# Kernel optimization log

Measured on AMD Instinct MI355X. Metric: run time of the kernel, lower is better.

## Reference

```python
import jax, jax.numpy as jnp
import numpy as np
import math

B, L, H, NH = 2, 256, 512, 8
DH = H // NH


def setup_inputs() -> dict:
    key0 = jax.random.key(0)
    ks = jax.random.split(key0, 20)
    s = 0.02
    inp = {
        "key": jax.random.normal(ks[0], (B, L, H), jnp.float32),
        "query": jax.random.normal(ks[1], (B, L, H), jnp.float32),
        "value": jax.random.normal(ks[2], (B, L, H), jnp.float32),
        "seq_len": L // 2 + jax.random.randint(ks[3], (B,), 0, L // 2 + 1),
        "lex_num": 0,
        "pos_s": jax.random.randint(ks[4], (B, L), 0, L),
        "pos_e": jax.random.randint(ks[5], (B, L), 0, L),
        "rel_pos_embedding": jax.random.normal(ks[6], (B, L, L, H), jnp.float32),
        "Wk": jax.random.normal(ks[7], (H, H), jnp.float32) * s,
        "bk": jnp.zeros((H,), jnp.float32),
        "Wq": jax.random.normal(ks[8], (H, H), jnp.float32) * s,
        "bq": jnp.zeros((H,), jnp.float32),
        "Wv": jax.random.normal(ks[9], (H, H), jnp.float32) * s,
        "bv": jnp.zeros((H,), jnp.float32),
        "Wr": jax.random.normal(ks[10], (H, H), jnp.float32) * s,
        "br": jnp.zeros((H,), jnp.float32),
        "u": jax.random.normal(ks[11], (NH, DH), jnp.float32) * s,
        "v": jax.random.normal(ks[12], (NH, DH), jnp.float32) * s,
        "Wf": jax.random.normal(ks[13], (H, H), jnp.float32) * s,
        "bf": jnp.zeros((H,), jnp.float32),
    }
    return inp


def reference(key, query, value, seq_len, lex_num, pos_s, pos_e, rel_pos_embedding,
              Wk, bk, Wq, bq, Wv, bv, Wr, br, u, v, Wf, bf):
    b, sl = key.shape[0], key.shape[1]
    # projections (k/q/v/r_proj all True)
    k = key @ Wk + bk
    q = query @ Wq + bq
    val = value @ Wv + bv
    rel = rel_pos_embedding @ Wr + br            # [B,L,L,H]
    # split heads
    kh = k.reshape(b, sl, NH, DH).transpose(0, 2, 1, 3)    # [B,nh,L,dh]
    qh = q.reshape(b, sl, NH, DH).transpose(0, 2, 1, 3)
    vh = val.reshape(b, sl, NH, DH).transpose(0, 2, 1, 3)
    relh = rel.reshape(b, sl, sl, NH, DH)                   # [B,L,L,nh,dh]
    # A+C: (q + u) @ k^T
    q_u = qh + u[None, :, None, :]
    AC = jnp.einsum('bnid,bnjd->bnij', q_u, kh)
    # B+D: (q + v) . rel_pos per (i,j) pair
    q_v = qh + v[None, :, None, :]
    BD = jnp.einsum('bnid,bijnd->bnij', q_v, relh)
    scores = (AC + BD) / math.sqrt(DH)
    # mask padded keys: mask[b,j] = j < seq_len[b] + lex_num
    valid = jnp.arange(sl)[None, :] < (seq_len + lex_num)[:, None]   # [B,L]
    scores = jnp.where(valid[:, None, None, :], scores, -1e15)
    attn = jax.nn.softmax(scores, axis=-1)       # dropout p=0 -> identity
    out = jnp.einsum('bnij,bnjd->bnid', attn, vh)
    out = out.transpose(0, 2, 1, 3).reshape(b, sl, H)
    return out @ Wf + bf
```

## Files before the change

### kernel.cpp

```cpp
#include <hip/hip_runtime.h>
#include <math.h>


__global__ __launch_bounds__(256) void gemm512_k(
    const float* __restrict__ A0, const float* __restrict__ W0,
    const float* __restrict__ b0, float* __restrict__ C0,
    const float* __restrict__ A1, const float* __restrict__ W1,
    const float* __restrict__ b1, float* __restrict__ C1,
    const float* __restrict__ A2, const float* __restrict__ W2,
    const float* __restrict__ b2, float* __restrict__ C2) {
  const int z = blockIdx.z;
  const float* A    = (z == 0) ? A0 : (z == 1) ? A1 : A2;
  const float* W    = (z == 0) ? W0 : (z == 1) ? W1 : W2;
  const float* bias = (z == 0) ? b0 : (z == 1) ? b1 : b2;
  float* C          = (z == 0) ? C0 : (z == 1) ? C1 : C2;

  __shared__ float As[16][64];
  __shared__ float Bs[16][64];
  const int t  = threadIdx.x;
  const int tx = t & 15, ty = t >> 4;
  const int bm0 = blockIdx.y * 64, bn0 = blockIdx.x * 64;
  const int lm  = t >> 2;
  const int lkq = (t & 3) << 2;
  const int lk  = t >> 4;
  const int lnq = (t & 15) << 2;

  float acc[4][4] = {};
  for (int kt = 0; kt < 32; ++kt) {
    float4 a4 = *(const float4*)&A[(bm0 + lm) * 512 + kt * 16 + lkq];
    float4 b4 = *(const float4*)&W[(kt * 16 + lk) * 512 + bn0 + lnq];
    As[lkq + 0][lm] = a4.x;
    As[lkq + 1][lm] = a4.y;
    As[lkq + 2][lm] = a4.z;
    As[lkq + 3][lm] = a4.w;
    *(float4*)&Bs[lk][lnq] = b4;
    __syncthreads();
#pragma unroll
    for (int k = 0; k < 16; ++k) {
      float4 av = *(const float4*)&As[k][ty * 4];
      float4 bv = *(const float4*)&Bs[k][tx * 4];
      acc[0][0] = fmaf(av.x, bv.x, acc[0][0]);
      acc[0][1] = fmaf(av.x, bv.y, acc[0][1]);
      acc[0][2] = fmaf(av.x, bv.z, acc[0][2]);
      acc[0][3] = fmaf(av.x, bv.w, acc[0][3]);
      acc[1][0] = fmaf(av.y, bv.x, acc[1][0]);
      acc[1][1] = fmaf(av.y, bv.y, acc[1][1]);
      acc[1][2] = fmaf(av.y, bv.z, acc[1][2]);
      acc[1][3] = fmaf(av.y, bv.w, acc[1][3]);
      acc[2][0] = fmaf(av.z, bv.x, acc[2][0]);
      acc[2][1] = fmaf(av.z, bv.y, acc[2][1]);
      acc[2][2] = fmaf(av.z, bv.z, acc[2][2]);
      acc[2][3] = fmaf(av.z, bv.w, acc[2][3]);
      acc[3][0] = fmaf(av.w, bv.x, acc[3][0]);
      acc[3][1] = fmaf(av.w, bv.y, acc[3][1]);
      acc[3][2] = fmaf(av.w, bv.z, acc[3][2]);
      acc[3][3] = fmaf(av.w, bv.w, acc[3][3]);
    }
    __syncthreads();
  }
  float4 bb = *(const float4*)&bias[bn0 + tx * 4];
#pragma unroll
  for (int r = 0; r < 4; ++r) {
    float4 o;
    o.x = acc[r][0] + bb.x;
    o.y = acc[r][1] + bb.y;
    o.z = acc[r][2] + bb.z;
    o.w = acc[r][3] + bb.w;
    *(float4*)&C[(size_t)(bm0 + ty * 4 + r) * 512 + bn0 + tx * 4] = o;
  }
}

__global__ __launch_bounds__(256) void g_gemm_k(const float* __restrict__ q,
                                                const float* __restrict__ vbias,
                                                const float* __restrict__ Wr,
                                                float* __restrict__ g) {
  __shared__ float As[64][64];
  __shared__ float Bs[64][64];
  const int t   = threadIdx.x;
  const int bi0 = blockIdx.x * 64;
  const int eb  = blockIdx.y * 64;
  const int n   = blockIdx.z;
  const int row = t >> 2;
  const int dq  = (t & 3) << 4;
#pragma unroll
  for (int s = 0; s < 4; ++s) {
    int d = dq + s * 4;
    float4 a4 = *(const float4*)&q[(size_t)(bi0 + row) * 512 + n * 64 + d];
    float4 v4 = *(const float4*)&vbias[n * 64 + d];
    As[d + 0][row] = a4.x + v4.x;
    As[d + 1][row] = a4.y + v4.y;
    As[d + 2][row] = a4.z + v4.z;
    As[d + 3][row] = a4.w + v4.w;
    float4 b4 = *(const float4*)&Wr[(size_t)(eb + row) * 512 + n * 64 + d];
    Bs[d + 0][row] = b4.x;
    Bs[d + 1][row] = b4.y;
    Bs[d + 2][row] = b4.z;
    Bs[d + 3][row] = b4.w;
  }
  __syncthreads();
  const int tx = t & 15, ty = t >> 4;
  float acc[4][4] = {};
#pragma unroll 8
  for (int d = 0; d < 64; ++d) {
    float4 av = *(const float4*)&As[d][ty * 4];
    float4 bv = *(const float4*)&Bs[d][tx * 4];
    acc[0][0] = fmaf(av.x, bv.x, acc[0][0]);
    acc[0][1] = fmaf(av.x, bv.y, acc[0][1]);
    acc[0][2] = fmaf(av.x, bv.z, acc[0][2]);
    acc[0][3] = fmaf(av.x, bv.w, acc[0][3]);
    acc[1][0] = fmaf(av.y, bv.x, acc[1][0]);
    acc[1][1] = fmaf(av.y, bv.y, acc[1][1]);
    acc[1][2] = fmaf(av.y, bv.z, acc[1][2]);
    acc[1][3] = fmaf(av.y, bv.w, acc[1][3]);
    acc[2][0] = fmaf(av.z, bv.x, acc[2][0]);
    acc[2][1] = fmaf(av.z, bv.y, acc[2][1]);
    acc[2][2] = fmaf(av.z, bv.z, acc[2][2]);
    acc[2][3] = fmaf(av.z, bv.w, acc[2][3]);
    acc[3][0] = fmaf(av.w, bv.x, acc[3][0]);
    acc[3][1] = fmaf(av.w, bv.y, acc[3][1]);
    acc[3][2] = fmaf(av.w, bv.z, acc[3][2]);
    acc[3][3] = fmaf(av.w, bv.w, acc[3][3]);
  }
#pragma unroll
  for (int r = 0; r < 4; ++r) {
    float4 o = {acc[r][0], acc[r][1], acc[r][2], acc[r][3]};
    *(float4*)&g[((size_t)(bi0 + ty * 4 + r) * 8 + n) * 512 + eb + tx * 4] = o;
  }
}

__global__ __launch_bounds__(256) void score_k(
    const float* __restrict__ q, const float* __restrict__ kk,
    const float* __restrict__ g, const float* __restrict__ rpe,
    const float* __restrict__ u, const float* __restrict__ v,
    const float* __restrict__ br, const int* __restrict__ seq_len,
    const int* __restrict__ lex_num, float* __restrict__ scores) {
  const int bi = blockIdx.x;
  const int b = bi >> 8, i = bi & 255;
  const int lane = threadIdx.x & 63;
  const int w = threadIdx.x >> 6;
  const int grp = lane >> 3, sub = lane & 7;
  const int e0 = lane << 3;
  const int jblock = blockIdx.y * 128;
  const int jbase = jblock + w * 32;
  __shared__ float ac[8][128];
  __shared__ float cterm[8];
  const int limit = seq_len[b] + lex_num[0];

  float qu[8];
  {
    const float* qrow = q + (size_t)bi * 512 + e0;
    float4 q0 = *(const float4*)qrow;
    float4 q1 = *(const float4*)(qrow + 4);
    float4 u0 = *(const float4*)(u + e0);
    float4 u1 = *(const float4*)(u + e0 + 4);
    qu[0] = q0.x + u0.x; qu[1] = q0.y + u0.y; qu[2] = q0.z + u0.z; qu[3] = q0.w + u0.w;
    qu[4] = q1.x + u1.x; qu[5] = q1.y + u1.y; qu[6] = q1.z + u1.z; qu[7] = q1.w + u1.w;
  }
  for (int jj = 0; jj < 32; ++jj) {
    int j = jbase + jj;
    const float* krow = kk + (size_t)(b * 256 + j) * 512 + e0;
    float4 k0 = *(const float4*)krow;
    float4 k1 = *(const float4*)(krow + 4);
    float p = qu[0] * k0.x;
    p = fmaf(qu[1], k0.y, p);
    p = fmaf(qu[2], k0.z, p);
    p = fmaf(qu[3], k0.w, p);
    p = fmaf(qu[4], k1.x, p);
    p = fmaf(qu[5], k1.y, p);
    p = fmaf(qu[6], k1.z, p);
    p = fmaf(qu[7], k1.w, p);
    p += __shfl_xor(p, 1);
    p += __shfl_xor(p, 2);
    p += __shfl_xor(p, 4);
    if (sub == 0) ac[grp][j - jblock] = p;
  }
  if (w == 0) {
    const float* qrow = q + (size_t)bi * 512 + e0;
    float4 q0 = *(const float4*)qrow;
    float4 q1 = *(const float4*)(qrow + 4);
    float4 v0 = *(const float4*)(v + e0);
    float4 v1 = *(const float4*)(v + e0 + 4);
    float4 r0 = *(const float4*)(br + e0);
    float4 r1 = *(const float4*)(br + e0 + 4);
    float p = (q0.x + v0.x) * r0.x;
    p = fmaf(q0.y + v0.y, r0.y, p);
    p = fmaf(q0.z + v0.z, r0.z, p);
    p = fmaf(q0.w + v0.w, r0.w, p);
    p = fmaf(q1.x + v1.x, r1.x, p);
    p = fmaf(q1.y + v1.y, r1.y, p);
    p = fmaf(q1.z + v1.z, r1.z, p);
    p = fmaf(q1.w + v1.w, r1.w, p);
    p += __shfl_xor(p, 1);
    p += __shfl_xor(p, 2);
    p += __shfl_xor(p, 4);
    if (sub == 0) cterm[grp] = p;
  }
  __syncthreads();

  float gf[8][8];
#pragma unroll
  for (int n = 0; n < 8; ++n) {
    const float* grow = g + ((size_t)bi * 8 + n) * 512 + e0;
    float4 ga = *(const float4*)grow;
    float4 gb = *(const float4*)(grow + 4);
    gf[n][0] = ga.x; gf[n][1] = ga.y; gf[n][2] = ga.z; gf[n][3] = ga.w;
    gf[n][4] = gb.x; gf[n][5] = gb.y; gf[n][6] = gb.z; gf[n][7] = gb.w;
  }
  const int s1 = sub & 1, s2 = (sub >> 1) & 1, s4 = (sub >> 2) & 1;
  const float* rbase = rpe + (size_t)bi * 256 * 512;
#pragma unroll 2
  for (int jj = 0; jj < 32; ++jj) {
    int j = jbase + jj;
    const float* rrow = rbase + (size_t)j * 512 + e0;
    float4 r0 = *(const float4*)rrow;
    float4 r1 = *(const float4*)(rrow + 4);
    float a[8];
#pragma unroll
    for (int n = 0; n < 8; ++n) {
      float s = r0.x * gf[n][0];
      s = fmaf(r0.y, gf[n][1], s);
      s = fmaf(r0.z, gf[n][2], s);
      s = fmaf(r0.w, gf[n][3], s);
      s = fmaf(r1.x, gf[n][4], s);
      s = fmaf(r1.y, gf[n][5], s);
      s = fmaf(r1.z, gf[n][6], s);
      s = fmaf(r1.w, gf[n][7], s);
      a[n] = s;
    }
    float b0 = (s1 ? a[1] : a[0]) + __shfl_xor(s1 ? a[0] : a[1], 1);
    float b1 = (s1 ? a[3] : a[2]) + __shfl_xor(s1 ? a[2] : a[3], 1);
    float b2 = (s1 ? a[5] : a[4]) + __shfl_xor(s1 ? a[4] : a[5], 1);
    float b3 = (s1 ? a[7] : a[6]) + __shfl_xor(s1 ? a[6] : a[7], 1);
    float c0 = (s2 ? b1 : b0) + __shfl_xor(s2 ? b0 : b1, 2);
    float c1 = (s2 ? b3 : b2) + __shfl_xor(s2 ? b2 : b3, 2);
    float tot = (s4 ? c1 : c0) + __shfl_xor(s4 ? c0 : c1, 4);
    tot += __shfl_xor(tot, 8);
    tot += __shfl_xor(tot, 16);
    tot += __shfl_xor(tot, 32);
    if (lane < 8) {
      float val = (ac[lane][j - jblock] + cterm[lane] + tot) * 0.125f;
      if (j >= limit) val = -1e15f;
      scores[((size_t)(b * 8 + lane) * 256 + i) * 256 + j] = val;
    }
  }
}

__global__ __launch_bounds__(256) void softmax_pv_k(const float* __restrict__ scores,
                                                    const float* __restrict__ val,
                                                    float* __restrict__ ctx) {
  const int bi = blockIdx.x;
  const int b = bi >> 8, i = bi & 255;
  const int t = threadIdx.x;
  const int lane = t & 63, w = t >> 6;
  __shared__ float p_lds[8][256];
#pragma unroll
  for (int h = 0; h < 2; ++h) {
    const int n = w * 2 + h;
    const float* srow = scores + ((size_t)(b * 8 + n) * 256 + i) * 256;
    float x0 = srow[lane], x1 = srow[lane + 64], x2 = srow[lane + 128], x3 = srow[lane + 192];
    float m = fmaxf(fmaxf(x0, x1), fmaxf(x2, x3));
#pragma unroll
    for (int off = 1; off < 64; off <<= 1) m = fmaxf(m, __shfl_xor(m, off));
    float e0 = __expf(x0 - m), e1 = __expf(x1 - m), e2 = __expf(x2 - m), e3 = __expf(x3 - m);
    float s = e0 + e1 + e2 + e3;
#pragma unroll
    for (int off = 1; off < 64; off <<= 1) s += __shfl_xor(s, off);
    float inv = 1.0f / s;
    p_lds[n][lane] = e0 * inv;
    p_lds[n][lane + 64] = e1 * inv;
    p_lds[n][lane + 128] = e2 * inv;
    p_lds[n][lane + 192] = e3 * inv;
  }
  __syncthreads();
  const int c = t * 2;
  const int n = c >> 6;
  float2 acc = {0.f, 0.f};
  const float* vb = val + (size_t)b * 256 * 512 + c;
#pragma unroll 4
  for (int j = 0; j < 256; ++j) {
    float p = p_lds[n][j];
    float2 vv = *(const float2*)(vb + (size_t)j * 512);
    acc.x = fmaf(p, vv.x, acc.x);
    acc.y = fmaf(p, vv.y, acc.y);
  }
  *(float2*)&ctx[(size_t)bi * 512 + c] = acc;
}

extern "C" void kernel_launch(void* const* d_in, const int* in_sizes, int n_in,
                              void* d_out, int out_size, void* d_ws, size_t ws_size,
                              hipStream_t stream) {
  const float* key     = (const float*)d_in[0];
  const float* query   = (const float*)d_in[1];
  const float* value   = (const float*)d_in[2];
  const int* seq_len   = (const int*)d_in[3];
  const int* lex_num   = (const int*)d_in[4];
  const float* rpe     = (const float*)d_in[7];
  const float* Wk      = (const float*)d_in[8];
  const float* bk      = (const float*)d_in[9];
  const float* Wq      = (const float*)d_in[10];
  const float* bq      = (const float*)d_in[11];
  const float* Wv      = (const float*)d_in[12];
  const float* bv      = (const float*)d_in[13];
  const float* Wr      = (const float*)d_in[14];
  const float* br      = (const float*)d_in[15];
  const float* u       = (const float*)d_in[16];
  const float* v       = (const float*)d_in[17];
  const float* Wf      = (const float*)d_in[18];
  const float* bf      = (const float*)d_in[19];
  float* out = (float*)d_out;

  float* ws     = (float*)d_ws;
  float* q_ws   = ws;
  float* k_ws   = q_ws + 262144;
  float* val_ws = k_ws + 262144;
  float* g_ws   = val_ws + 262144;
  float* sc_ws  = g_ws + 2097152;
  float* ctx_ws = sc_ws + 1048576;

  dim3 blk(256);
  gemm512_k<<<dim3(8, 8, 3), blk, 0, stream>>>(query, Wq, bq, q_ws,
                                               key, Wk, bk, k_ws,
                                               value, Wv, bv, val_ws);
  g_gemm_k<<<dim3(8, 8, 8), blk, 0, stream>>>(q_ws, v, Wr, g_ws);
  score_k<<<dim3(512, 2), blk, 0, stream>>>(q_ws, k_ws, g_ws, rpe, u, v, br,
                                            seq_len, lex_num, sc_ws);
  softmax_pv_k<<<dim3(512), blk, 0, stream>>>(sc_ws, val_ws, ctx_ws);
  gemm512_k<<<dim3(8, 8, 1), blk, 0, stream>>>(ctx_ws, Wf, bf, out,
                                               ctx_ws, Wf, bf, out,
                                               ctx_ws, Wf, bf, out);
}
```

Measured before the change: 530.4 us.

## Fuse score, softmax and PV into one attention kernel; prefetch GEMM tiles

The score kernel and the softmax-PV kernel are merged into a single attn_k kernel per (b,i) row. Scores stay in shared memory instead of going out to global, and the q·k term is folded into the rel-pos reduction per head. The grid shrinks from 512x2 to 512 blocks, each handling all 256 keys, so there is less parallelism on the dominant rel_pos_embedding stream. The projection GEMM also register-prefetches the next k tile so global loads overlap the FMA loop.

```diff
diff --git a/kernel.cpp b/kernel.cpp
--- a/kernel.cpp
+++ b/kernel.cpp
@@ -26,15 +26,20 @@
   const int lnq = (t & 15) << 2;
 
   float acc[4][4] = {};
+  float4 a4 = *(const float4*)&A[(bm0 + lm) * 512 + lkq];
+  float4 b4 = *(const float4*)&W[lk * 512 + bn0 + lnq];
   for (int kt = 0; kt < 32; ++kt) {
-    float4 a4 = *(const float4*)&A[(bm0 + lm) * 512 + kt * 16 + lkq];
-    float4 b4 = *(const float4*)&W[(kt * 16 + lk) * 512 + bn0 + lnq];
     As[lkq + 0][lm] = a4.x;
     As[lkq + 1][lm] = a4.y;
     As[lkq + 2][lm] = a4.z;
     As[lkq + 3][lm] = a4.w;
     *(float4*)&Bs[lk][lnq] = b4;
     __syncthreads();
+    float4 a4n = a4, b4n = b4;
+    if (kt < 31) {
+      a4n = *(const float4*)&A[(bm0 + lm) * 512 + (kt + 1) * 16 + lkq];
+      b4n = *(const float4*)&W[((kt + 1) * 16 + lk) * 512 + bn0 + lnq];
+    }
 #pragma unroll
     for (int k = 0; k < 16; ++k) {
       float4 av = *(const float4*)&As[k][ty * 4];
@@ -57,6 +62,8 @@
       acc[3][3] = fmaf(av.w, bv.w, acc[3][3]);
     }
     __syncthreads();
+    a4 = a4n;
+    b4 = b4n;
   }
   float4 bb = *(const float4*)&bias[bn0 + tx * 4];
 #pragma unroll
@@ -128,21 +135,20 @@
   }
 }
 
-__global__ __launch_bounds__(256) void score_k(
+__global__ __launch_bounds__(256) void attn_k(
     const float* __restrict__ q, const float* __restrict__ kk,
     const float* __restrict__ g, const float* __restrict__ rpe,
     const float* __restrict__ u, const float* __restrict__ v,
     const float* __restrict__ br, const int* __restrict__ seq_len,
-    const int* __restrict__ lex_num, float* __restrict__ scores) {
+    const int* __restrict__ lex_num, const float* __restrict__ val,
+    float* __restrict__ ctx) {
   const int bi = blockIdx.x;
-  const int b = bi >> 8, i = bi & 255;
-  const int lane = threadIdx.x & 63;
-  const int w = threadIdx.x >> 6;
+  const int b = bi >> 8;
+  const int t = threadIdx.x;
+  const int lane = t & 63, w = t >> 6;
   const int grp = lane >> 3, sub = lane & 7;
   const int e0 = lane << 3;
-  const int jblock = blockIdx.y * 128;
-  const int jbase = jblock + w * 32;
-  __shared__ float ac[8][128];
+  __shared__ float sc[8][256];
   __shared__ float cterm[8];
   const int limit = seq_len[b] + lex_num[0];
 
@@ -156,23 +162,14 @@
     qu[0] = q0.x + u0.x; qu[1] = q0.y + u0.y; qu[2] = q0.z + u0.z; qu[3] = q0.w + u0.w;
     qu[4] = q1.x + u1.x; qu[5] = q1.y + u1.y; qu[6] = q1.z + u1.z; qu[7] = q1.w + u1.w;
   }
-  for (int jj = 0; jj < 32; ++jj) {
-    int j = jbase + jj;
-    const float* krow = kk + (size_t)(b * 256 + j) * 512 + e0;
-    float4 k0 = *(const float4*)krow;
-    float4 k1 = *(const float4*)(krow + 4);
-    float p = qu[0] * k0.x;
-    p = fmaf(qu[1], k0.y, p);
-    p = fmaf(qu[2], k0.z, p);
-    p = fmaf(qu[3], k0.w, p);
-    p = fmaf(qu[4], k1.x, p);
-    p = fmaf(qu[5], k1.y, p);
-    p = fmaf(qu[6], k1.z, p);
-    p = fmaf(qu[7], k1.w, p);
-    p += __shfl_xor(p, 1);
-    p += __shfl_xor(p, 2);
-    p += __shfl_xor(p, 4);
-    if (sub == 0) ac[grp][j - jblock] = p;
+  float gf[8][8];
+#pragma unroll
+  for (int n = 0; n < 8; ++n) {
+    const float* grow = g + ((size_t)bi * 8 + n) * 512 + e0;
+    float4 ga = *(const float4*)grow;
+    float4 gb = *(const float4*)(grow + 4);
+    gf[n][0] = ga.x; gf[n][1] = ga.y; gf[n][2] = ga.z; gf[n][3] = ga.w;
+    gf[n][4] = gb.x; gf[n][5] = gb.y; gf[n][6] = gb.z; gf[n][7] = gb.w;
   }
   if (w == 0) {
     const float* qrow = q + (size_t)bi * 512 + e0;
@@ -197,23 +194,26 @@
   }
   __syncthreads();
 
-  float gf[8][8];
-#pragma unroll
-  for (int n = 0; n < 8; ++n) {
-    const float* grow = g + ((size_t)bi * 8 + n) * 512 + e0;
-    float4 ga = *(const float4*)grow;
-    float4 gb = *(const float4*)(grow + 4);
-    gf[n][0] = ga.x; gf[n][1] = ga.y; gf[n][2] = ga.z; gf[n][3] = ga.w;
-    gf[n][4] = gb.x; gf[n][5] = gb.y; gf[n][6] = gb.z; gf[n][7] = gb.w;
-  }
   const int s1 = sub & 1, s2 = (sub >> 1) & 1, s4 = (sub >> 2) & 1;
   const float* rbase = rpe + (size_t)bi * 256 * 512;
+  const float* kbase = kk + (size_t)b * 256 * 512;
 #pragma unroll 2
-  for (int jj = 0; jj < 32; ++jj) {
-    int j = jbase + jj;
+  for (int jj = 0; jj < 64; ++jj) {
+    const int j = w * 64 + jj;
     const float* rrow = rbase + (size_t)j * 512 + e0;
+    const float* krow = kbase + (size_t)j * 512 + e0;
     float4 r0 = *(const float4*)rrow;
     float4 r1 = *(const float4*)(rrow + 4);
+    float4 k0 = *(const float4*)krow;
+    float4 k1 = *(const float4*)(krow + 4);
+    float kd = qu[0] * k0.x;
+    kd = fmaf(qu[1], k0.y, kd);
+    kd = fmaf(qu[2], k0.z, kd);
+    kd = fmaf(qu[3], k0.w, kd);
+    kd = fmaf(qu[4], k1.x, kd);
+    kd = fmaf(qu[5], k1.y, kd);
+    kd = fmaf(qu[6], k1.z, kd);
+    kd = fmaf(qu[7], k1.w, kd);
     float a[8];
 #pragma unroll
     for (int n = 0; n < 8; ++n) {
@@ -225,7 +225,7 @@
       s = fmaf(r1.y, gf[n][5], s);
       s = fmaf(r1.z, gf[n][6], s);
       s = fmaf(r1.w, gf[n][7], s);
-      a[n] = s;
+      a[n] = s + ((grp == n) ? kd : 0.0f);
     }
     float b0 = (s1 ? a[1] : a[0]) + __shfl_xor(s1 ? a[0] : a[1], 1);
     float b1 = (s1 ? a[3] : a[2]) + __shfl_xor(s1 ? a[2] : a[3], 1);
@@ -238,52 +238,48 @@
     tot += __shfl_xor(tot, 16);
     tot += __shfl_xor(tot, 32);
     if (lane < 8) {
-      float val = (ac[lane][j - jblock] + cterm[lane] + tot) * 0.125f;
-      if (j >= limit) val = -1e15f;
-      scores[((size_t)(b * 8 + lane) * 256 + i) * 256 + j] = val;
+      float sval = (tot + cterm[lane]) * 0.125f;
+      if (j >= limit) sval = -1e15f;
+      sc[lane][j] = sval;
     }
   }
-}
-
-__global__ __launch_bounds__(256) void softmax_pv_k(const float* __restrict__ scores,
-                                                    const float* __restrict__ val,
-                                                    float* __restrict__ ctx) {
-  const int bi = blockIdx.x;
-  const int b = bi >> 8, i = bi & 255;
-  const int t = threadIdx.x;
-  const int lane = t & 63, w = t >> 6;
-  __shared__ float p_lds[8][256];
+  __syncthreads();
+
 #pragma unroll
   for (int h = 0; h < 2; ++h) {
     const int n = w * 2 + h;
-    const float* srow = scores + ((size_t)(b * 8 + n) * 256 + i) * 256;
-    float x0 = srow[lane], x1 = srow[lane + 64], x2 = srow[lane + 128], x3 = srow[lane + 192];
+    float x0 = sc[n][lane], x1 = sc[n][lane + 64];
+    float x2 = sc[n][lane + 128], x3 = sc[n][lane + 192];
     float m = fmaxf(fmaxf(x0, x1), fmaxf(x2, x3));
 #pragma unroll
     for (int off = 1; off < 64; off <<= 1) m = fmaxf(m, __shfl_xor(m, off));
-    float e0 = __expf(x0 - m), e1 = __expf(x1 - m), e2 = __expf(x2 - m), e3 = __expf(x3 - m);
-    float s = e0 + e1 + e2 + e3;
+    float e0v = __expf(x0 - m), e1v = __expf(x1 - m);
+    float e2v = __expf(x2 - m), e3v = __expf(x3 - m);
+    float s = e0v + e1v + e2v + e3v;
 #pragma unroll
     for (int off = 1; off < 64; off <<= 1) s += __shfl_xor(s, off);
     float inv = 1.0f / s;
-    p_lds[n][lane] = e0 * inv;
-    p_lds[n][lane + 64] = e1 * inv;
-    p_lds[n][lane + 128] = e2 * inv;
-    p_lds[n][lane + 192] = e3 * inv;
+    sc[n][lane] = e0v * inv;
+    sc[n][lane + 64] = e1v * inv;
+    sc[n][lane + 128] = e2v * inv;
+    sc[n][lane + 192] = e3v * inv;
   }
   __syncthreads();
+
   const int c = t * 2;
   const int n = c >> 6;
   float2 acc = {0.f, 0.f};
   const float* vb = val + (size_t)b * 256 * 512 + c;
 #pragma unroll 4
   for (int j = 0; j < 256; ++j) {
-    float p = p_lds[n][j];
+    float p = sc[n][j];
     float2 vv = *(const float2*)(vb + (size_t)j * 512);
     acc.x = fmaf(p, vv.x, acc.x);
     acc.y = fmaf(p, vv.y, acc.y);
   }
-  *(float2*)&ctx[(size_t)bi * 512 + c] = acc;
+  float* crow = ctx + (size_t)bi * 512 + c;
+  crow[0] = acc.x;
+  crow[1] = acc.y;
 }
 
 extern "C" void kernel_launch(void* const* d_in, const int* in_sizes, int n_in,
@@ -314,17 +310,15 @@
   float* k_ws   = q_ws + 262144;
   float* val_ws = k_ws + 262144;
   float* g_ws   = val_ws + 262144;
-  float* sc_ws  = g_ws + 2097152;
-  float* ctx_ws = sc_ws + 1048576;
+  float* ctx_ws = g_ws + 2097152;
 
   dim3 blk(256);
   gemm512_k<<<dim3(8, 8, 3), blk, 0, stream>>>(query, Wq, bq, q_ws,
                                                key, Wk, bk, k_ws,
                                                value, Wv, bv, val_ws);
   g_gemm_k<<<dim3(8, 8, 8), blk, 0, stream>>>(q_ws, v, Wr, g_ws);
-  score_k<<<dim3(512, 2), blk, 0, stream>>>(q_ws, k_ws, g_ws, rpe, u, v, br,
-                                            seq_len, lex_num, sc_ws);
-  softmax_pv_k<<<dim3(512), blk, 0, stream>>>(sc_ws, val_ws, ctx_ws);
+  attn_k<<<dim3(512), blk, 0, stream>>>(q_ws, k_ws, g_ws, rpe, u, v, br,
+                                        seq_len, lex_num, val_ws, ctx_ws);
   gemm512_k<<<dim3(8, 8, 1), blk, 0, stream>>>(ctx_ws, Wf, bf, out,
                                                ctx_ws, Wf, bf, out,
                                                ctx_ws, Wf, bf, out);
```

New measurement: 475.4 us. 10.4% less time.
